# Optimization experiments

Measured on AMD Instinct MI355X. Metric: run time of the kernel, lower is better.

## Reference

```python
import jax, jax.numpy as jnp
import numpy as np

U, DP, TOPK, NH = 2, 16, 8, 2
D = 512
M = DP ** U          # 256 slots
DK = U * DP          # 32 addressing dim
BETA_MAX = 2.0


def setup_inputs():
    key = jax.random.key(0)
    ks = jax.random.split(key, 12)
    B, T = 8, 128
    s = 0.02
    return {
        "h": jax.random.normal(ks[0], (B, T, D), jnp.float32),
        "K_slots": jax.random.normal(ks[1], (B, M, D), jnp.float32) * s,
        "V_slots": jax.random.normal(ks[2], (B, M, D), jnp.float32) * s,
        "z_K": jnp.ones((B, M), jnp.float32),
        "z_V": jnp.ones((B, M), jnp.float32),
        "W_k": jax.random.normal(ks[3], (DK, D), jnp.float32) * s,
        "W_q": jax.random.normal(ks[4], (DK, D), jnp.float32) * s,
        "log_tau_w": jnp.zeros((1,), jnp.float32),
        "log_tau_r": jnp.zeros((1,), jnp.float32),
        "hh_k": jax.random.normal(ks[5], (NH, D, D), jnp.float32) * s,
        "hh_vk": jax.random.normal(ks[6], (NH, D, D), jnp.float32) * s,
        "hh_vv": jax.random.normal(ks[7], (NH, D, D), jnp.float32) * s,
        "hh_bw": jax.random.normal(ks[8], (NH, 1, D), jnp.float32) * s,
        "hh_bb": jnp.zeros((NH, 1), jnp.float32),
        "gamma": jnp.float32(1.0),
        "W_out": jax.random.normal(ks[9], (D, D), jnp.float32) * s,
        "W_gate": jax.random.normal(ks[10], (D, D), jnp.float32) * s,
    }


def _kron_address(z, log_tau):
    # z: [B, DK]; Kronecker-factored softmax address over M = DP**U slots
    B = z.shape[0]
    probs = jax.nn.softmax(z.reshape(B, U, DP) / jnp.exp(log_tau[0]), axis=-1)
    addr = probs[:, 0]
    for u in range(1, U):
        addr = (addr[:, :, None] * probs[:, u, None, :]).reshape(B, -1)
    w, idx = jax.lax.top_k(addr, TOPK)
    return idx, w


def _forward(h, K_slots, V_slots, z_K, z_V, W_k, W_q, log_tau_w, log_tau_r,
             hh_k, hh_vk, hh_vv, hh_bw, hh_bb, gamma, W_out, W_gate,
             checkpoint=False):
    B, T, _ = h.shape
    scale = D ** -0.5
    b_idx = jnp.arange(B)[:, None]
    sp_gamma = jax.nn.softplus(gamma)

    def step(carry, h_t):
        K_s, V_s, zK, zV = carry
        write_idx, write_w = _kron_address(h_t @ W_k.T, log_tau_w)
        read_idx, _ = _kron_address(h_t @ W_q.T, log_tau_r)
        # scatter write weights into dense [B, M] (top-k indices are unique)
        w_full = jnp.zeros((B, M), h_t.dtype).at[b_idx, write_idx].set(write_w)
        # PDMA decay
        decay = (1.0 - w_full) ** sp_gamma
        K_s = decay[..., None] * K_s
        V_s = decay[..., None] * V_s
        zK = decay * zK + w_full
        zV = decay * zV + w_full
        # gather active slots: [B, K, D]
        K_act = jnp.take_along_axis(K_s, write_idx[:, :, None], axis=1)
        V_act = jnp.take_along_axis(V_s, write_idx[:, :, None], axis=1)
        # Householder update chain
        for j in range(NH):
            k_j = jax.nn.silu(h_t @ hh_k[j].T)
            k_hat = k_j / jnp.maximum(
                jnp.linalg.norm(k_j, axis=-1, keepdims=True), 1e-12)
            v_kj = h_t @ hh_vk[j].T
            v_vj = h_t @ hh_vv[j].T
            beta = BETA_MAX * jax.nn.sigmoid(h_t @ hh_bw[j].T + hh_bb[j])  # [B,1]
            kh = k_hat[:, None, :]
            be = beta[:, None, :]
            K_act = K_act - be * kh * (kh * K_act).sum(-1, keepdims=True) \
                    + be * k_j[:, None, :] * v_kj[:, None, :]
            V_act = V_act - be * kh * (kh * V_act).sum(-1, keepdims=True) \
                    + be * k_j[:, None, :] * v_vj[:, None, :]
        # scatter updated slots back
        K_s = K_s.at[b_idx, write_idx].set(K_act)
        V_s = V_s.at[b_idx, write_idx].set(V_act)
        # read path
        K_read = jnp.take_along_axis(K_s, read_idx[:, :, None], axis=1)
        V_read = jnp.take_along_axis(V_s, read_idx[:, :, None], axis=1)
        zK_read = jnp.take_along_axis(zK, read_idx, axis=1)[..., None]
        zV_read = jnp.take_along_axis(zV, read_idx, axis=1)[..., None]
        K_n = K_read / zK_read
        V_n = V_read / zV_read
        rel = (K_n * h_t[:, None, :]).sum(-1)           # [B, K]
        attn = jax.nn.softmax(rel * scale, axis=-1)
        readout = (attn[..., None] * V_n).sum(1)        # [B, D]
        out = jax.nn.sigmoid(h_t @ W_gate.T) * (readout @ W_out.T)
        return (K_s, V_s, zK, zV), (out, write_idx, read_idx)

    step_fn = jax.checkpoint(step) if checkpoint else step
    (K_s, V_s, zK, zV), (outs, widx, ridx) = jax.lax.scan(
        step_fn, (K_slots, V_slots, z_K, z_V), jnp.swapaxes(h, 0, 1))
    return (jnp.swapaxes(outs, 0, 1), K_s, V_s, zK, zV, widx[-1], ridx[-1])


def reference(h, K_slots, V_slots, z_K, z_V, W_k, W_q, log_tau_w, log_tau_r,
              hh_k, hh_vk, hh_vv, hh_bw, hh_bb, gamma, W_out, W_gate):
    return _forward(h, K_slots, V_slots, z_K, z_V, W_k, W_q, log_tau_w,
                    log_tau_r, hh_k, hh_vk, hh_vv, hh_bw, hh_bb, gamma,
                    W_out, W_gate)
```

## Files before the change

kernel.cpp:

```cpp
#include <hip/hip_runtime.h>
#include <math.h>

#define D_ 512
#define M_ 256
#define T_ 128
#define B_ 8
#define TOPK_ 8
#define NH_ 2
#define BT_ (B_*T_)

__device__ __forceinline__ float wred(float v){
#pragma unroll
  for (int m = 1; m < 64; m <<= 1) v += __shfl_xor(v, m, 64);
  return v;
}
__device__ __forceinline__ float4 ld4(const float* p){ return *(const float4*)p; }
__device__ __forceinline__ void st4(float* p, float4 v){ *(float4*)p = v; }
__device__ __forceinline__ float dot4(float4 a, float4 b){
  return a.x*b.x + a.y*b.y + a.z*b.z + a.w*b.w;
}
__device__ __forceinline__ float4 scl4(float4 a, float s){
  a.x*=s; a.y*=s; a.z*=s; a.w*=s; return a;
}

template<int CTRL>
__device__ __forceinline__ float dpp_add(float x){
  int y = __builtin_amdgcn_update_dpp(0, __float_as_int(x), CTRL, 0xf, 0xf, true);
  return x + __int_as_float(y);
}
__device__ __forceinline__ float wredd(float x){
  x = dpp_add<0x111>(x);
  x = dpp_add<0x112>(x);
  x = dpp_add<0x114>(x);
  x = dpp_add<0x118>(x);
  x = dpp_add<0x142>(x);
  x = dpp_add<0x143>(x);
  return __int_as_float(__builtin_amdgcn_readlane(__float_as_int(x), 63));
}

__global__ __launch_bounds__(64) void addr_kernel(
    const float* __restrict__ h, const float* __restrict__ Wk,
    const float* __restrict__ Wq, const float* __restrict__ ltw,
    const float* __restrict__ ltr, const float* __restrict__ gammap,
    float* __restrict__ metab)
{
  const int bt = blockIdx.x;
  const int tid = threadIdx.x;
  __shared__ float p_s[64];

  const float* hrow = h + (size_t)bt*D_;
  const float* wrow = (tid < 32) ? (Wk + (size_t)tid*D_)
                                 : (Wq + (size_t)(tid-32)*D_);
  float dot = 0.f;
  for (int d = 0; d < D_; d += 4){
    float4 hv = ld4(&hrow[d]); float4 wv = ld4(&wrow[d]);
    dot += hv.x*wv.x + hv.y*wv.y + hv.z*wv.z + hv.w*wv.w;
  }
  float tau = (tid < 32) ? expf(ltw[0]) : expf(ltr[0]);
  float mx = dot;
#pragma unroll
  for (int m = 1; m < 16; m <<= 1) mx = fmaxf(mx, __shfl_xor(mx, m, 64));
  float e = expf((dot - mx)/tau);
  float sm = e;
#pragma unroll
  for (int m = 1; m < 16; m <<= 1) sm += __shfl_xor(sm, m, 64);
  p_s[tid] = e / sm;
  __syncthreads();

  const int half = tid >> 5;
  const int l = tid & 31;
  const int g0 = half*32, g1 = half*32 + 16;
  float av[8];
#pragma unroll
  for (int k = 0; k < 8; ++k){
    int x = l*8 + k;
    av[k] = p_s[g0 + (x>>4)] * p_s[g1 + (x&15)];
  }
  const float sp = log1pf(expf(gammap[0]));
  for (int r = 0; r < TOPK_; ++r){
    float bv = -1.f; int bi = 0;
#pragma unroll
    for (int k = 0; k < 8; ++k){ if (av[k] > bv){ bv = av[k]; bi = l*8+k; } }
#pragma unroll
    for (int m = 1; m < 32; m <<= 1){
      float ov = __shfl_xor(bv, m, 64); int oi = __shfl_xor(bi, m, 64);
      if (ov > bv || (ov == bv && oi < bi)){ bv = ov; bi = oi; }
    }
    if ((bi >> 3) == l) av[bi & 7] = -2.f;
    float* mp = metab + (size_t)(bt*TOPK_ + r)*4;
    if (tid == 0){
      mp[0] = __int_as_float(bi); mp[1] = bv; mp[2] = powf(1.f - bv, sp);
    }
    if (tid == 32) mp[3] = __int_as_float(bi);
  }
}

struct GemmPtrs { const float* W[6]; float* C[6]; };

__global__ __launch_bounds__(256) void gemm_nt(
    const float* __restrict__ A, GemmPtrs p,
    const float* __restrict__ zK0, const float* __restrict__ zV0,
    const float* __restrict__ metab, float2* __restrict__ zr,
    float* __restrict__ o_zK, float* __restrict__ o_zV)
{
  if (blockIdx.z == 6){
    if (blockIdx.y != 0) return;
    const int b = blockIdx.x;
    const int m = threadIdx.x;
    const float4* mb = (const float4*)metab + (size_t)b*T_*TOPK_;
    float zk = zK0[b*M_+m], zv = zV0[b*M_+m];
    float4 cur[TOPK_];
#pragma unroll
    for (int i = 0; i < TOPK_; ++i) cur[i] = mb[i];
    for (int t = 0; t < T_; ++t){
      const float4* src = mb + ((t+1 < T_) ? (t+1)*TOPK_ : t*TOPK_);
      float4 nxt[TOPK_];
#pragma unroll
      for (int i = 0; i < TOPK_; ++i) nxt[i] = src[i];
#pragma unroll
      for (int i = 0; i < TOPK_; ++i){
        bool hit = (m == __float_as_int(cur[i].x));
        float nzk = cur[i].z*zk + cur[i].y;
        float nzv = cur[i].z*zv + cur[i].y;
        zk = hit ? nzk : zk;
        zv = hit ? nzv : zv;
      }
#pragma unroll
      for (int i = 0; i < TOPK_; ++i){
        if (m == __float_as_int(cur[i].w))
          zr[(size_t)(b*T_+t)*TOPK_+i] =
              make_float2(1.0f/zk, 1.0f/zv);
      }
#pragma unroll
      for (int i = 0; i < TOPK_; ++i) cur[i] = nxt[i];
    }
    o_zK[b*M_+m] = zk; o_zV[b*M_+m] = zv;
    return;
  }

  const float* W = p.W[blockIdx.z];
  float* C = p.C[blockIdx.z];
  const int n0 = blockIdx.x * 64;
  const int m0 = blockIdx.y * 64;
  const int tid = threadIdx.x;
  __shared__ __align__(16) float As[2][16][68];
  __shared__ __align__(16) float Bs[2][16][68];
  const int r  = tid >> 2;
  const int c4 = (tid & 3) << 2;
  const int tx4 = (tid & 15) << 2;
  const int ty4 = (tid >> 4) << 2;
  float acc[4][4] = {{0.f}};

  {
    float4 av = ld4(&A[(size_t)(m0+r)*512 + c4]);
    float4 wv = ld4(&W[(size_t)(n0+r)*512 + c4]);
    As[0][c4+0][r]=av.x; As[0][c4+1][r]=av.y; As[0][c4+2][r]=av.z; As[0][c4+3][r]=av.w;
    Bs[0][c4+0][r]=wv.x; Bs[0][c4+1][r]=wv.y; Bs[0][c4+2][r]=wv.z; Bs[0][c4+3][r]=wv.w;
  }
  __syncthreads();

  for (int kc = 0, buf = 0; kc < 512; kc += 16, buf ^= 1){
    float4 av, wv;
    const bool more = (kc + 16 < 512);
    if (more){
      av = ld4(&A[(size_t)(m0+r)*512 + kc + 16 + c4]);
      wv = ld4(&W[(size_t)(n0+r)*512 + kc + 16 + c4]);
    }
#pragma unroll
    for (int k = 0; k < 16; ++k){
      float4 a  = ld4(&As[buf][k][ty4]);
      float4 bq = ld4(&Bs[buf][k][tx4]);
      acc[0][0]+=a.x*bq.x; acc[0][1]+=a.x*bq.y; acc[0][2]+=a.x*bq.z; acc[0][3]+=a.x*bq.w;
      acc[1][0]+=a.y*bq.x; acc[1][1]+=a.y*bq.y; acc[1][2]+=a.y*bq.z; acc[1][3]+=a.y*bq.w;
      acc[2][0]+=a.z*bq.x; acc[2][1]+=a.z*bq.y; acc[2][2]+=a.z*bq.z; acc[2][3]+=a.z*bq.w;
      acc[3][0]+=a.w*bq.x; acc[3][1]+=a.w*bq.y; acc[3][2]+=a.w*bq.z; acc[3][3]+=a.w*bq.w;
    }
    if (more){
      int nb = buf ^ 1;
      As[nb][c4+0][r]=av.x; As[nb][c4+1][r]=av.y; As[nb][c4+2][r]=av.z; As[nb][c4+3][r]=av.w;
      Bs[nb][c4+0][r]=wv.x; Bs[nb][c4+1][r]=wv.y; Bs[nb][c4+2][r]=wv.z; Bs[nb][c4+3][r]=wv.w;
      __syncthreads();
    }
  }
#pragma unroll
  for (int i = 0; i < 4; ++i){
    float4 cv; cv.x=acc[i][0]; cv.y=acc[i][1]; cv.z=acc[i][2]; cv.w=acc[i][3];
    st4(&C[(size_t)(m0+ty4+i)*512 + n0 + tx4], cv);
  }
}

__global__ __launch_bounds__(256) void gemm_out(
    const float* __restrict__ h, const float* __restrict__ rdo,
    const float* __restrict__ Wg, const float* __restrict__ Wo,
    float* __restrict__ C)
{
  const int n0 = blockIdx.x * 64;
  const int m0 = blockIdx.y * 64;
  const int tid = threadIdx.x;
  __shared__ __align__(16) float Ag[16][68];
  __shared__ __align__(16) float Ao[16][68];
  __shared__ __align__(16) float Bg[16][68];
  __shared__ __align__(16) float Bo[16][68];
  const int r  = tid >> 2;
  const int c4 = (tid & 3) << 2;
  const int tx4 = (tid & 15) << 2;
  const int ty4 = (tid >> 4) << 2;
  float accg[4][4] = {{0.f}};
  float acco[4][4] = {{0.f}};

  for (int kc = 0; kc < 512; kc += 16){
    float4 a1 = ld4(&h  [(size_t)(m0+r)*512 + kc + c4]);
    float4 a2 = ld4(&rdo[(size_t)(m0+r)*512 + kc + c4]);
    float4 w1 = ld4(&Wg [(size_t)(n0+r)*512 + kc + c4]);
    float4 w2 = ld4(&Wo [(size_t)(n0+r)*512 + kc + c4]);
    __syncthreads();
    Ag[c4+0][r]=a1.x; Ag[c4+1][r]=a1.y; Ag[c4+2][r]=a1.z; Ag[c4+3][r]=a1.w;
    Ao[c4+0][r]=a2.x; Ao[c4+1][r]=a2.y; Ao[c4+2][r]=a2.z; Ao[c4+3][r]=a2.w;
    Bg[c4+0][r]=w1.x; Bg[c4+1][r]=w1.y; Bg[c4+2][r]=w1.z; Bg[c4+3][r]=w1.w;
    Bo[c4+0][r]=w2.x; Bo[c4+1][r]=w2.y; Bo[c4+2][r]=w2.z; Bo[c4+3][r]=w2.w;
    __syncthreads();
#pragma unroll
    for (int k = 0; k < 16; ++k){
      float4 ag = ld4(&Ag[k][ty4]);
      float4 ao = ld4(&Ao[k][ty4]);
      float4 bg = ld4(&Bg[k][tx4]);
      float4 bo = ld4(&Bo[k][tx4]);
      accg[0][0]+=ag.x*bg.x; accg[0][1]+=ag.x*bg.y; accg[0][2]+=ag.x*bg.z; accg[0][3]+=ag.x*bg.w;
      accg[1][0]+=ag.y*bg.x; accg[1][1]+=ag.y*bg.y; accg[1][2]+=ag.y*bg.z; accg[1][3]+=ag.y*bg.w;
      accg[2][0]+=ag.z*bg.x; accg[2][1]+=ag.z*bg.y; accg[2][2]+=ag.z*bg.z; accg[2][3]+=ag.z*bg.w;
      accg[3][0]+=ag.w*bg.x; accg[3][1]+=ag.w*bg.y; accg[3][2]+=ag.w*bg.z; accg[3][3]+=ag.w*bg.w;
      acco[0][0]+=ao.x*bo.x; acco[0][1]+=ao.x*bo.y; acco[0][2]+=ao.x*bo.z; acco[0][3]+=ao.x*bo.w;
      acco[1][0]+=ao.y*bo.x; acco[1][1]+=ao.y*bo.y; acco[1][2]+=ao.y*bo.z; acco[1][3]+=ao.y*bo.w;
      acco[2][0]+=ao.z*bo.x; acco[2][1]+=ao.z*bo.y; acco[2][2]+=ao.z*bo.z; acco[2][3]+=ao.z*bo.w;
      acco[3][0]+=ao.w*bo.x; acco[3][1]+=ao.w*bo.y; acco[3][2]+=ao.w*bo.z; acco[3][3]+=ao.w*bo.w;
    }
  }
#pragma unroll
  for (int i = 0; i < 4; ++i){
    float4 cv;
    cv.x = acco[i][0] / (1.f + expf(-accg[i][0]));
    cv.y = acco[i][1] / (1.f + expf(-accg[i][1]));
    cv.z = acco[i][2] / (1.f + expf(-accg[i][2]));
    cv.w = acco[i][3] / (1.f + expf(-accg[i][3]));
    st4(&C[(size_t)(m0+ty4+i)*512 + n0 + tx4], cv);
  }
}

__global__ __launch_bounds__(256) void ew2_kernel(
    float* __restrict__ khat, float* __restrict__ kvk, float* __restrict__ kvv,
    float* __restrict__ pre2, const float* __restrict__ h,
    const float* __restrict__ hh_bw, const float* __restrict__ hh_bb)
{
  const int bt = blockIdx.x;
  const int tid = threadIdx.x;
  const int wid = tid >> 6, lane = tid & 63;
  float* k0p  = khat + (size_t)bt*D_;
  float* k1p  = khat + (size_t)BT_*D_ + (size_t)bt*D_;
  float* vk0p = kvk  + (size_t)bt*D_;
  float* vk1p = kvk  + (size_t)BT_*D_ + (size_t)bt*D_;
  float* vv0p = kvv  + (size_t)bt*D_;
  float* vv1p = kvv  + (size_t)BT_*D_ + (size_t)bt*D_;
  const float* hp  = h + (size_t)bt*D_;

  float s0[2], s1[2];
  float n0 = 0.f, n1 = 0.f, bd0 = 0.f, bd1 = 0.f;
#pragma unroll
  for (int q = 0; q < 2; ++q){
    int d = tid + q*256;
    float x0 = k0p[d], x1 = k1p[d], hv = hp[d];
    float v0 = x0 / (1.f + expf(-x0));
    float v1 = x1 / (1.f + expf(-x1));
    s0[q] = v0; s1[q] = v1;
    n0 += v0*v0; n1 += v1*v1;
    bd0 += hv*hh_bw[d]; bd1 += hv*hh_bw[D_ + d];
  }
  __shared__ float4 rb[4];
  float4 acc = make_float4(wred(n0), wred(n1), wred(bd0), wred(bd1));
  if (lane == 0) rb[wid] = acc;
  __syncthreads();
  float4 t0 = rb[0], t1 = rb[1], t2 = rb[2], t3 = rb[3];
  n0 = t0.x+t1.x+t2.x+t3.x; n1 = t0.y+t1.y+t2.y+t3.y;
  bd0 = t0.z+t1.z+t2.z+t3.z; bd1 = t0.w+t1.w+t2.w+t3.w;
  float inv0 = 1.f / fmaxf(sqrtf(n0), 1e-12f);
  float inv1 = 1.f / fmaxf(sqrtf(n1), 1e-12f);
  float be0 = 2.f / (1.f + expf(-(bd0 + hh_bb[0])));
  float be1 = 2.f / (1.f + expf(-(bd1 + hh_bb[1])));

  float c01 = 0.f, dK = 0.f, dV = 0.f;
#pragma unroll
  for (int q = 0; q < 2; ++q){
    int d = tid + q*256;
    float kh0 = s0[q]*inv0, kh1 = s1[q]*inv1;
    float u0K = s0[q]*vk0p[d], u1K = s1[q]*vk1p[d];
    float u0V = s0[q]*vv0p[d], u1V = s1[q]*vv1p[d];
    k0p[d] = kh0; k1p[d] = kh1;
    vk0p[d] = be0*u0K + be1*u1K;
    vv0p[d] = be0*u0V + be1*u1V;
    c01 += kh1*kh0; dK += kh1*u0K; dV += kh1*u0V;
  }
  __syncthreads();
  float4 acc2 = make_float4(wred(c01), wred(dK), wred(dV), 0.f);
  if (lane == 0) rb[wid] = acc2;
  __syncthreads();
  if (tid == 0){
    float4 a = rb[0], b = rb[1], c = rb[2], d = rb[3];
    pre2[(size_t)bt*8+0] = a.x+b.x+c.x+d.x;
    pre2[(size_t)bt*8+1] = a.y+b.y+c.y+d.y;
    pre2[(size_t)bt*8+2] = a.z+b.z+c.z+d.z;
    pre2[(size_t)bt*8+3] = be0;
    pre2[(size_t)bt*8+4] = be1;
  }
}

__global__ __launch_bounds__(512) void scan_kernel(
    float* __restrict__ Ks, float* __restrict__ Vs,
    const float* __restrict__ khat, const float* __restrict__ ucKp,
    const float* __restrict__ ucVp, const float* __restrict__ pre2,
    const float* __restrict__ metab, const float2* __restrict__ zr,
    const float* __restrict__ h, float* __restrict__ readout,
    float* __restrict__ o_widx, float* __restrict__ o_ridx)
{
  __shared__ __align__(16) float Vr_s[2][TOPK_][D_];
  __shared__ float2 rel2_s[2][TOPK_];

  const int b = blockIdx.x;
  const int tid = threadIdx.x;
  const int s = tid >> 6, lane = tid & 63;
  const int l4 = lane * 4;
  const float scale = 0.044194173824159216f;

  float* Ksb = Ks + (size_t)b*M_*D_;
  float* Vsb = Vs + (size_t)b*M_*D_;
  const float* kh0p = khat;
  const float* kh1p = khat + (size_t)BT_*D_;
  const float4* mb = (const float4*)metab;

  const int bt0 = b*T_;
  size_t o0 = (size_t)bt0*D_ + l4;
  float4 c_kh0a = ld4(kh0p+o0), c_kh0b = ld4(kh0p+o0+256);
  float4 c_kh1a = ld4(kh1p+o0), c_kh1b = ld4(kh1p+o0+256);
  float4 c_uKa  = ld4(ucKp+o0), c_uKb  = ld4(ucKp+o0+256);
  float4 c_uVa  = ld4(ucVp+o0), c_uVb  = ld4(ucVp+o0+256);

  float4 me   = mb[bt0*TOPK_ + s];
  float4 me_n = mb[(bt0+1)*TOPK_ + s];
  float4 pm   = ld4(&pre2[(size_t)bt0*8]);
  float  be1v = pre2[(size_t)bt0*8+4];
  float4 pm_n = ld4(&pre2[(size_t)(bt0+1)*8]);
  float  be1_n= pre2[(size_t)(bt0+1)*8+4];
  float2 zr2   = zr[(size_t)bt0*TOPK_ + s];
  float2 zr2_n = zr[(size_t)(bt0+1)*TOPK_ + s];

  int mi = __float_as_int(me.x);
  float4 K0 = ld4(&Ksb[(size_t)mi*D_ + l4]);
  float4 K1 = ld4(&Ksb[(size_t)mi*D_ + 256 + l4]);
  float4 V0 = ld4(&Vsb[(size_t)mi*D_ + l4]);
  float4 V1 = ld4(&Vsb[(size_t)mi*D_ + 256 + l4]);

#pragma unroll 2
  for (int t = 0; t < T_; ++t){
    const int bt = b*T_ + t;
    const float dec = me.z;
    const int   ri  = __float_as_int(me.w);
    mi = __float_as_int(me.x);

    const int btn  = (t+1 < T_) ? bt+1 : bt;
    const int btnn = (t+2 < T_) ? bt+2 : b*T_+T_-1;
    size_t on = (size_t)btn*D_ + l4;
    float4 n_kh0a = ld4(kh0p+on), n_kh0b = ld4(kh0p+on+256);
    float4 n_kh1a = ld4(kh1p+on), n_kh1b = ld4(kh1p+on+256);
    float4 n_uKa  = ld4(ucKp+on), n_uKb  = ld4(ucKp+on+256);
    float4 n_uVa  = ld4(ucVp+on), n_uVb  = ld4(ucVp+on+256);
    float4 HTa = ld4(h + (size_t)bt*D_ + l4);
    float4 HTb = ld4(h + (size_t)bt*D_ + 256 + l4);
    float4 me_nn = mb[btnn*TOPK_ + s];
    float4 pm_nn = ld4(&pre2[(size_t)btnn*8]);
    float  be1nn = pre2[(size_t)btnn*8+4];
    float2 zr2nn = zr[(size_t)btnn*TOPK_ + s];

    K0 = scl4(K0,dec); K1 = scl4(K1,dec);
    V0 = scl4(V0,dec); V1 = scl4(V1,dec);
    float aK = wredd(dot4(K0,c_kh0a) + dot4(K1,c_kh0b));
    float bK = wredd(dot4(K0,c_kh1a) + dot4(K1,c_kh1b));
    float aV = wredd(dot4(V0,c_kh0a) + dot4(V1,c_kh0b));
    float bV = wredd(dot4(V0,c_kh1a) + dot4(V1,c_kh1b));
    float p0K = pm.w*aK, p1K = be1v*(bK + pm.w*(pm.y - aK*pm.x));
    float p0V = pm.w*aV, p1V = be1v*(bV + pm.w*(pm.z - aV*pm.x));
    K0.x += c_uKa.x - p0K*c_kh0a.x - p1K*c_kh1a.x;
    K0.y += c_uKa.y - p0K*c_kh0a.y - p1K*c_kh1a.y;
    K0.z += c_uKa.z - p0K*c_kh0a.z - p1K*c_kh1a.z;
    K0.w += c_uKa.w - p0K*c_kh0a.w - p1K*c_kh1a.w;
    K1.x += c_uKb.x - p0K*c_kh0b.x - p1K*c_kh1b.x;
    K1.y += c_uKb.y - p0K*c_kh0b.y - p1K*c_kh1b.y;
    K1.z += c_uKb.z - p0K*c_kh0b.z - p1K*c_kh1b.z;
    K1.w += c_uKb.w - p0K*c_kh0b.w - p1K*c_kh1b.w;
    V0.x += c_uVa.x - p0V*c_kh0a.x - p1V*c_kh1a.x;
    V0.y += c_uVa.y - p0V*c_kh0a.y - p1V*c_kh1a.y;
    V0.z += c_uVa.z - p0V*c_kh0a.z - p1V*c_kh1a.z;
    V0.w += c_uVa.w - p0V*c_kh0a.w - p1V*c_kh1a.w;
    V1.x += c_uVb.x - p0V*c_kh0b.x - p1V*c_kh1b.x;
    V1.y += c_uVb.y - p0V*c_kh0b.y - p1V*c_kh1b.y;
    V1.z += c_uVb.z - p0V*c_kh0b.z - p1V*c_kh1b.z;
    V1.w += c_uVb.w - p0V*c_kh0b.w - p1V*c_kh1b.w;

    st4(&Ksb[(size_t)mi*D_ + l4], K0); st4(&Ksb[(size_t)mi*D_ + 256 + l4], K1);
    st4(&Vsb[(size_t)mi*D_ + l4], V0); st4(&Vsb[(size_t)mi*D_ + 256 + l4], V1);

    __syncthreads();

    float4 RK0 = ld4(&Ksb[(size_t)ri*D_ + l4]);
    float4 RK1 = ld4(&Ksb[(size_t)ri*D_ + 256 + l4]);
    float4 RV0 = ld4(&Vsb[(size_t)ri*D_ + l4]);
    float4 RV1 = ld4(&Vsb[(size_t)ri*D_ + 256 + l4]);
    const int mi_n = __float_as_int(me_n.x);
    float4 nK0 = ld4(&Ksb[(size_t)mi_n*D_ + l4]);
    float4 nK1 = ld4(&Ksb[(size_t)mi_n*D_ + 256 + l4]);
    float4 nV0 = ld4(&Vsb[(size_t)mi_n*D_ + l4]);
    float4 nV1 = ld4(&Vsb[(size_t)mi_n*D_ + 256 + l4]);

    if (t > 0){
      const int pp = (t-1) & 1;
      float2 rz[TOPK_];
#pragma unroll
      for (int i = 0; i < TOPK_; ++i) rz[i] = rel2_s[pp][i];
      float mx = rz[0].x;
#pragma unroll
      for (int i = 1; i < TOPK_; ++i) mx = fmaxf(mx, rz[i].x);
      float smm = 0.f, r = 0.f;
#pragma unroll
      for (int i = 0; i < TOPK_; ++i){
        float ev = __expf(rz[i].x - mx); smm += ev;
        r += ev * rz[i].y * Vr_s[pp][i][tid];
      }
      readout[(size_t)(bt-1)*D_ + tid] = r * __builtin_amdgcn_rcpf(smm);
    }

    float dt = wredd(dot4(RK0,HTa) + dot4(RK1,HTb));
    if (lane == 0)
      rel2_s[t&1][s] = make_float2(dt * scale * zr2.x, zr2.y);
    st4(&Vr_s[t&1][s][l4], RV0); st4(&Vr_s[t&1][s][256+l4], RV1);

    K0=nK0; K1=nK1; V0=nV0; V1=nV1;
    me=me_n; pm=pm_n; be1v=be1_n; zr2=zr2_n;
    me_n=me_nn; pm_n=pm_nn; be1_n=be1nn; zr2_n=zr2nn;
    c_kh0a=n_kh0a; c_kh0b=n_kh0b; c_kh1a=n_kh1a; c_kh1b=n_kh1b;
    c_uKa=n_uKa; c_uKb=n_uKb; c_uVa=n_uVa; c_uVb=n_uVb;
  }

  __syncthreads();
  {
    const int btL = b*T_ + T_ - 1;
    const int pp = (T_-1) & 1;
    float2 rz[TOPK_];
#pragma unroll
    for (int i = 0; i < TOPK_; ++i) rz[i] = rel2_s[pp][i];
    float mx = rz[0].x;
#pragma unroll
    for (int i = 1; i < TOPK_; ++i) mx = fmaxf(mx, rz[i].x);
    float smm = 0.f, r = 0.f;
#pragma unroll
    for (int i = 0; i < TOPK_; ++i){
      float ev = __expf(rz[i].x - mx); smm += ev;
      r += ev * rz[i].y * Vr_s[pp][i][tid];
    }
    readout[(size_t)btL*D_ + tid] = r * __builtin_amdgcn_rcpf(smm);

    if (tid < TOPK_){
      float4 m = mb[btL*TOPK_ + tid];
      o_widx[b*TOPK_+tid] = (float)__float_as_int(m.x);
      o_ridx[b*TOPK_+tid] = (float)__float_as_int(m.w);
    }
  }
}

extern "C" void kernel_launch(void* const* d_in, const int* in_sizes, int n_in,
                              void* d_out, int out_size, void* d_ws, size_t ws_size,
                              hipStream_t stream)
{
  (void)in_sizes; (void)n_in; (void)out_size; (void)ws_size;
  const float* h       = (const float*)d_in[0];
  const float* K_slots = (const float*)d_in[1];
  const float* V_slots = (const float*)d_in[2];
  const float* z_K     = (const float*)d_in[3];
  const float* z_V     = (const float*)d_in[4];
  const float* W_k     = (const float*)d_in[5];
  const float* W_q     = (const float*)d_in[6];
  const float* ltw     = (const float*)d_in[7];
  const float* ltr     = (const float*)d_in[8];
  const float* hh_k    = (const float*)d_in[9];
  const float* hh_vk   = (const float*)d_in[10];
  const float* hh_vv   = (const float*)d_in[11];
  const float* hh_bw   = (const float*)d_in[12];
  const float* hh_bb   = (const float*)d_in[13];
  const float* gamma   = (const float*)d_in[14];
  const float* W_out   = (const float*)d_in[15];
  const float* W_gate  = (const float*)d_in[16];

  float* out    = (float*)d_out;
  float* o_outs = out;
  float* o_Ks   = out + 524288;
  float* o_Vs   = out + 1572864;
  float* o_zK   = out + 2621440;
  float* o_zV   = out + 2623488;
  float* o_widx = out + 2625536;
  float* o_ridx = out + 2625600;

  float* ws    = (float*)d_ws;
  float* khat  = ws;
  float* kvk   = ws + 2*(size_t)BT_*D_;
  float* kvv   = kvk + 2*(size_t)BT_*D_;
  float* rdo   = kvv + 2*(size_t)BT_*D_;
  float* metab = rdo + (size_t)BT_*D_;
  float* pre2  = metab + (size_t)BT_*TOPK_*4;
  float2* zrb  = (float2*)(pre2 + (size_t)BT_*8);

  (void)hipMemcpyAsync(o_Ks, K_slots, sizeof(float)*(size_t)B_*M_*D_,
                       hipMemcpyDeviceToDevice, stream);
  (void)hipMemcpyAsync(o_Vs, V_slots, sizeof(float)*(size_t)B_*M_*D_,
                       hipMemcpyDeviceToDevice, stream);

  addr_kernel<<<BT_, 64, 0, stream>>>(h, W_k, W_q, ltw, ltr, gamma, metab);

  GemmPtrs p{};
  p.W[0] = hh_k;           p.C[0] = khat;
  p.W[1] = hh_k + 262144;  p.C[1] = khat + (size_t)BT_*D_;
  p.W[2] = hh_vk;          p.C[2] = kvk;
  p.W[3] = hh_vk + 262144; p.C[3] = kvk + (size_t)BT_*D_;
  p.W[4] = hh_vv;          p.C[4] = kvv;
  p.W[5] = hh_vv + 262144; p.C[5] = kvv + (size_t)BT_*D_;
  gemm_nt<<<dim3(8,16,7), 256, 0, stream>>>(h, p, z_K, z_V, metab, zrb,
                                            o_zK, o_zV);

  ew2_kernel<<<BT_, 256, 0, stream>>>(khat, kvk, kvv, pre2, h, hh_bw, hh_bb);

  scan_kernel<<<B_, 512, 0, stream>>>(o_Ks, o_Vs, khat, kvk, kvv,
                                      pre2, metab, zrb, h, rdo,
                                      o_widx, o_ridx);

  gemm_out<<<dim3(8,16), 256, 0, stream>>>(h, rdo, W_gate, W_out, o_outs);
}
```

Measured before the change: 464.1 us.

## Use bf16 MFMA for projection GEMMs and scalarize slot indices in scan

Replaces the shared-memory FP32 tiled GEMMs (gemm_nt and the fused gate/output gemm_out) with direct-from-global loads converted to bf16 and fed to 16x16x32 MFMA instructions, one wave per 16-column strip. It also remaps the z-recurrence block to index batch by blockIdx.y and uses readfirstlane to make per-warp slot indices scalar in the recurrent scan. The goal is to offload GEMM FLOPs to matrix cores and cut VGPR address arithmetic, at the cost of bf16 rounding of inputs and uncoalesced, non-reused global loads.

```diff
diff --git a/kernel.cpp b/kernel.cpp
--- a/kernel.cpp
+++ b/kernel.cpp
@@ -9,6 +9,9 @@
 #define NH_ 2
 #define BT_ (B_*T_)
 
+typedef __attribute__((ext_vector_type(8))) short bf8_t;
+typedef __attribute__((ext_vector_type(4))) float f4_t;
+
 __device__ __forceinline__ float wred(float v){
 #pragma unroll
   for (int m = 1; m < 64; m <<= 1) v += __shfl_xor(v, m, 64);
@@ -21,6 +24,19 @@
 }
 __device__ __forceinline__ float4 scl4(float4 a, float s){
   a.x*=s; a.y*=s; a.z*=s; a.w*=s; return a;
+}
+
+__device__ __forceinline__ short f2bf(float f){
+  unsigned u = __float_as_uint(f);
+  u += 0x7FFFu + ((u >> 16) & 1u);
+  return (short)(u >> 16);
+}
+__device__ __forceinline__ bf8_t cvt_frag(const float* p){
+  float4 x0 = ld4(p), x1 = ld4(p + 4);
+  bf8_t r;
+  r[0]=f2bf(x0.x); r[1]=f2bf(x0.y); r[2]=f2bf(x0.z); r[3]=f2bf(x0.w);
+  r[4]=f2bf(x1.x); r[5]=f2bf(x1.y); r[6]=f2bf(x1.z); r[7]=f2bf(x1.w);
+  return r;
 }
 
 template<int CTRL>
@@ -104,8 +120,8 @@
     float* __restrict__ o_zK, float* __restrict__ o_zV)
 {
   if (blockIdx.z == 6){
-    if (blockIdx.y != 0) return;
-    const int b = blockIdx.x;
+    if (blockIdx.x != 0 || blockIdx.y >= B_) return;
+    const int b = blockIdx.y;
     const int m = threadIdx.x;
     const float4* mb = (const float4*)metab + (size_t)b*T_*TOPK_;
     float zk = zK0[b*M_+m], zv = zV0[b*M_+m];
@@ -128,8 +144,7 @@
 #pragma unroll
       for (int i = 0; i < TOPK_; ++i){
         if (m == __float_as_int(cur[i].w))
-          zr[(size_t)(b*T_+t)*TOPK_+i] =
-              make_float2(1.0f/zk, 1.0f/zv);
+          zr[(size_t)(b*T_+t)*TOPK_+i] = make_float2(1.0f/zk, 1.0f/zv);
       }
 #pragma unroll
       for (int i = 0; i < TOPK_; ++i) cur[i] = nxt[i];
@@ -143,49 +158,40 @@
   const int n0 = blockIdx.x * 64;
   const int m0 = blockIdx.y * 64;
   const int tid = threadIdx.x;
-  __shared__ __align__(16) float As[2][16][68];
-  __shared__ __align__(16) float Bs[2][16][68];
-  const int r  = tid >> 2;
-  const int c4 = (tid & 3) << 2;
-  const int tx4 = (tid & 15) << 2;
-  const int ty4 = (tid >> 4) << 2;
-  float acc[4][4] = {{0.f}};
-
-  {
-    float4 av = ld4(&A[(size_t)(m0+r)*512 + c4]);
-    float4 wv = ld4(&W[(size_t)(n0+r)*512 + c4]);
-    As[0][c4+0][r]=av.x; As[0][c4+1][r]=av.y; As[0][c4+2][r]=av.z; As[0][c4+3][r]=av.w;
-    Bs[0][c4+0][r]=wv.x; Bs[0][c4+1][r]=wv.y; Bs[0][c4+2][r]=wv.z; Bs[0][c4+3][r]=wv.w;
-  }
-  __syncthreads();
-
-  for (int kc = 0, buf = 0; kc < 512; kc += 16, buf ^= 1){
-    float4 av, wv;
-    const bool more = (kc + 16 < 512);
-    if (more){
-      av = ld4(&A[(size_t)(m0+r)*512 + kc + 16 + c4]);
-      wv = ld4(&W[(size_t)(n0+r)*512 + kc + 16 + c4]);
-    }
-#pragma unroll
-    for (int k = 0; k < 16; ++k){
-      float4 a  = ld4(&As[buf][k][ty4]);
-      float4 bq = ld4(&Bs[buf][k][tx4]);
-      acc[0][0]+=a.x*bq.x; acc[0][1]+=a.x*bq.y; acc[0][2]+=a.x*bq.z; acc[0][3]+=a.x*bq.w;
-      acc[1][0]+=a.y*bq.x; acc[1][1]+=a.y*bq.y; acc[1][2]+=a.y*bq.z; acc[1][3]+=a.y*bq.w;
-      acc[2][0]+=a.z*bq.x; acc[2][1]+=a.z*bq.y; acc[2][2]+=a.z*bq.z; acc[2][3]+=a.z*bq.w;
-      acc[3][0]+=a.w*bq.x; acc[3][1]+=a.w*bq.y; acc[3][2]+=a.w*bq.z; acc[3][3]+=a.w*bq.w;
-    }
-    if (more){
-      int nb = buf ^ 1;
-      As[nb][c4+0][r]=av.x; As[nb][c4+1][r]=av.y; As[nb][c4+2][r]=av.z; As[nb][c4+3][r]=av.w;
-      Bs[nb][c4+0][r]=wv.x; Bs[nb][c4+1][r]=wv.y; Bs[nb][c4+2][r]=wv.z; Bs[nb][c4+3][r]=wv.w;
-      __syncthreads();
-    }
-  }
-#pragma unroll
-  for (int i = 0; i < 4; ++i){
-    float4 cv; cv.x=acc[i][0]; cv.y=acc[i][1]; cv.z=acc[i][2]; cv.w=acc[i][3];
-    st4(&C[(size_t)(m0+ty4+i)*512 + n0 + tx4], cv);
+  const int w = tid >> 6, lane = tid & 63;
+  const int mr = lane & 15, q = lane >> 4;
+
+  const float* a0p = A + (size_t)(m0 + mr)*512;
+  const float* a1p = a0p + (size_t)16*512;
+  const float* a2p = a1p + (size_t)16*512;
+  const float* a3p = a2p + (size_t)16*512;
+  const float* bp  = W + (size_t)(n0 + 16*w + mr)*512;
+
+  f4_t acc0 = {0.f,0.f,0.f,0.f}, acc1 = {0.f,0.f,0.f,0.f};
+  f4_t acc2 = {0.f,0.f,0.f,0.f}, acc3 = {0.f,0.f,0.f,0.f};
+
+#pragma unroll 2
+  for (int kc = 0; kc < 512; kc += 32){
+    const int ko = kc + q*8;
+    bf8_t bf = cvt_frag(bp + ko);
+    bf8_t af0 = cvt_frag(a0p + ko);
+    bf8_t af1 = cvt_frag(a1p + ko);
+    bf8_t af2 = cvt_frag(a2p + ko);
+    bf8_t af3 = cvt_frag(a3p + ko);
+    acc0 = __builtin_amdgcn_mfma_f32_16x16x32_bf16(af0, bf, acc0, 0, 0, 0);
+    acc1 = __builtin_amdgcn_mfma_f32_16x16x32_bf16(af1, bf, acc1, 0, 0, 0);
+    acc2 = __builtin_amdgcn_mfma_f32_16x16x32_bf16(af2, bf, acc2, 0, 0, 0);
+    acc3 = __builtin_amdgcn_mfma_f32_16x16x32_bf16(af3, bf, acc3, 0, 0, 0);
+  }
+
+  const int col = n0 + 16*w + mr;
+  float* c0 = C + (size_t)(m0 + q*4)*512 + col;
+#pragma unroll
+  for (int r = 0; r < 4; ++r){
+    c0[(size_t)r*512]            = acc0[r];
+    c0[(size_t)(16 + r)*512]     = acc1[r];
+    c0[(size_t)(32 + r)*512]     = acc2[r];
+    c0[(size_t)(48 + r)*512]     = acc3[r];
   }
 }
 
@@ -197,52 +203,43 @@
   const int n0 = blockIdx.x * 64;
   const int m0 = blockIdx.y * 64;
   const int tid = threadIdx.x;
-  __shared__ __align__(16) float Ag[16][68];
-  __shared__ __align__(16) float Ao[16][68];
-  __shared__ __align__(16) float Bg[16][68];
-  __shared__ __align__(16) float Bo[16][68];
-  const int r  = tid >> 2;
-  const int c4 = (tid & 3) << 2;
-  const int tx4 = (tid & 15) << 2;
-  const int ty4 = (tid >> 4) << 2;
-  float accg[4][4] = {{0.f}};
-  float acco[4][4] = {{0.f}};
-
-  for (int kc = 0; kc < 512; kc += 16){
-    float4 a1 = ld4(&h  [(size_t)(m0+r)*512 + kc + c4]);
-    float4 a2 = ld4(&rdo[(size_t)(m0+r)*512 + kc + c4]);
-    float4 w1 = ld4(&Wg [(size_t)(n0+r)*512 + kc + c4]);
-    float4 w2 = ld4(&Wo [(size_t)(n0+r)*512 + kc + c4]);
-    __syncthreads();
-    Ag[c4+0][r]=a1.x; Ag[c4+1][r]=a1.y; Ag[c4+2][r]=a1.z; Ag[c4+3][r]=a1.w;
-    Ao[c4+0][r]=a2.x; Ao[c4+1][r]=a2.y; Ao[c4+2][r]=a2.z; Ao[c4+3][r]=a2.w;
-    Bg[c4+0][r]=w1.x; Bg[c4+1][r]=w1.y; Bg[c4+2][r]=w1.z; Bg[c4+3][r]=w1.w;
-    Bo[c4+0][r]=w2.x; Bo[c4+1][r]=w2.y; Bo[c4+2][r]=w2.z; Bo[c4+3][r]=w2.w;
-    __syncthreads();
-#pragma unroll
-    for (int k = 0; k < 16; ++k){
-      float4 ag = ld4(&Ag[k][ty4]);
-      float4 ao = ld4(&Ao[k][ty4]);
-      float4 bg = ld4(&Bg[k][tx4]);
-      float4 bo = ld4(&Bo[k][tx4]);
-      accg[0][0]+=ag.x*bg.x; accg[0][1]+=ag.x*bg.y; accg[0][2]+=ag.x*bg.z; accg[0][3]+=ag.x*bg.w;
-      accg[1][0]+=ag.y*bg.x; accg[1][1]+=ag.y*bg.y; accg[1][2]+=ag.y*bg.z; accg[1][3]+=ag.y*bg.w;
-      accg[2][0]+=ag.z*bg.x; accg[2][1]+=ag.z*bg.y; accg[2][2]+=ag.z*bg.z; accg[2][3]+=ag.z*bg.w;
-      accg[3][0]+=ag.w*bg.x; accg[3][1]+=ag.w*bg.y; accg[3][2]+=ag.w*bg.z; accg[3][3]+=ag.w*bg.w;
-      acco[0][0]+=ao.x*bo.x; acco[0][1]+=ao.x*bo.y; acco[0][2]+=ao.x*bo.z; acco[0][3]+=ao.x*bo.w;
-      acco[1][0]+=ao.y*bo.x; acco[1][1]+=ao.y*bo.y; acco[1][2]+=ao.y*bo.z; acco[1][3]+=ao.y*bo.w;
-      acco[2][0]+=ao.z*bo.x; acco[2][1]+=ao.z*bo.y; acco[2][2]+=ao.z*bo.z; acco[2][3]+=ao.z*bo.w;
-      acco[3][0]+=ao.w*bo.x; acco[3][1]+=ao.w*bo.y; acco[3][2]+=ao.w*bo.z; acco[3][3]+=ao.w*bo.w;
-    }
-  }
+  const int w = tid >> 6, lane = tid & 63;
+  const int mr = lane & 15, q = lane >> 4;
+
+  const float* hp[4];  const float* op[4];
 #pragma unroll
   for (int i = 0; i < 4; ++i){
-    float4 cv;
-    cv.x = acco[i][0] / (1.f + expf(-accg[i][0]));
-    cv.y = acco[i][1] / (1.f + expf(-accg[i][1]));
-    cv.z = acco[i][2] / (1.f + expf(-accg[i][2]));
-    cv.w = acco[i][3] / (1.f + expf(-accg[i][3]));
-    st4(&C[(size_t)(m0+ty4+i)*512 + n0 + tx4], cv);
+    hp[i] = h   + (size_t)(m0 + 16*i + mr)*512;
+    op[i] = rdo + (size_t)(m0 + 16*i + mr)*512;
+  }
+  const float* gp = Wg + (size_t)(n0 + 16*w + mr)*512;
+  const float* wp = Wo + (size_t)(n0 + 16*w + mr)*512;
+
+  f4_t g[4], o[4];
+#pragma unroll
+  for (int i = 0; i < 4; ++i){ g[i] = (f4_t){0.f,0.f,0.f,0.f}; o[i] = (f4_t){0.f,0.f,0.f,0.f}; }
+
+#pragma unroll 2
+  for (int kc = 0; kc < 512; kc += 32){
+    const int ko = kc + q*8;
+    bf8_t bg = cvt_frag(gp + ko);
+    bf8_t bo = cvt_frag(wp + ko);
+#pragma unroll
+    for (int i = 0; i < 4; ++i){
+      bf8_t ah = cvt_frag(hp[i] + ko);
+      bf8_t ao = cvt_frag(op[i] + ko);
+      g[i] = __builtin_amdgcn_mfma_f32_16x16x32_bf16(ah, bg, g[i], 0, 0, 0);
+      o[i] = __builtin_amdgcn_mfma_f32_16x16x32_bf16(ao, bo, o[i], 0, 0, 0);
+    }
+  }
+
+  const int col = n0 + 16*w + mr;
+#pragma unroll
+  for (int i = 0; i < 4; ++i){
+    float* cp = C + (size_t)(m0 + 16*i + q*4)*512 + col;
+#pragma unroll
+    for (int r = 0; r < 4; ++r)
+      cp[(size_t)r*512] = o[i][r] / (1.f + expf(-g[i][r]));
   }
 }
 
@@ -351,100 +348,102 @@
   float2 zr2   = zr[(size_t)bt0*TOPK_ + s];
   float2 zr2_n = zr[(size_t)(bt0+1)*TOPK_ + s];
 
-  int mi = __float_as_int(me.x);
-  float4 K0 = ld4(&Ksb[(size_t)mi*D_ + l4]);
-  float4 K1 = ld4(&Ksb[(size_t)mi*D_ + 256 + l4]);
-  float4 V0 = ld4(&Vsb[(size_t)mi*D_ + l4]);
-  float4 V1 = ld4(&Vsb[(size_t)mi*D_ + 256 + l4]);
+  {
+    int mi0 = __builtin_amdgcn_readfirstlane(__float_as_int(me.x));
+    float4 K0 = ld4(&Ksb[(size_t)mi0*D_ + l4]);
+    float4 K1 = ld4(&Ksb[(size_t)mi0*D_ + 256 + l4]);
+    float4 V0 = ld4(&Vsb[(size_t)mi0*D_ + l4]);
+    float4 V1 = ld4(&Vsb[(size_t)mi0*D_ + 256 + l4]);
 
 #pragma unroll 2
-  for (int t = 0; t < T_; ++t){
-    const int bt = b*T_ + t;
-    const float dec = me.z;
-    const int   ri  = __float_as_int(me.w);
-    mi = __float_as_int(me.x);
-
-    const int btn  = (t+1 < T_) ? bt+1 : bt;
-    const int btnn = (t+2 < T_) ? bt+2 : b*T_+T_-1;
-    size_t on = (size_t)btn*D_ + l4;
-    float4 n_kh0a = ld4(kh0p+on), n_kh0b = ld4(kh0p+on+256);
-    float4 n_kh1a = ld4(kh1p+on), n_kh1b = ld4(kh1p+on+256);
-    float4 n_uKa  = ld4(ucKp+on), n_uKb  = ld4(ucKp+on+256);
-    float4 n_uVa  = ld4(ucVp+on), n_uVb  = ld4(ucVp+on+256);
-    float4 HTa = ld4(h + (size_t)bt*D_ + l4);
-    float4 HTb = ld4(h + (size_t)bt*D_ + 256 + l4);
-    float4 me_nn = mb[btnn*TOPK_ + s];
-    float4 pm_nn = ld4(&pre2[(size_t)btnn*8]);
-    float  be1nn = pre2[(size_t)btnn*8+4];
-    float2 zr2nn = zr[(size_t)btnn*TOPK_ + s];
-
-    K0 = scl4(K0,dec); K1 = scl4(K1,dec);
-    V0 = scl4(V0,dec); V1 = scl4(V1,dec);
-    float aK = wredd(dot4(K0,c_kh0a) + dot4(K1,c_kh0b));
-    float bK = wredd(dot4(K0,c_kh1a) + dot4(K1,c_kh1b));
-    float aV = wredd(dot4(V0,c_kh0a) + dot4(V1,c_kh0b));
-    float bV = wredd(dot4(V0,c_kh1a) + dot4(V1,c_kh1b));
-    float p0K = pm.w*aK, p1K = be1v*(bK + pm.w*(pm.y - aK*pm.x));
-    float p0V = pm.w*aV, p1V = be1v*(bV + pm.w*(pm.z - aV*pm.x));
-    K0.x += c_uKa.x - p0K*c_kh0a.x - p1K*c_kh1a.x;
-    K0.y += c_uKa.y - p0K*c_kh0a.y - p1K*c_kh1a.y;
-    K0.z += c_uKa.z - p0K*c_kh0a.z - p1K*c_kh1a.z;
-    K0.w += c_uKa.w - p0K*c_kh0a.w - p1K*c_kh1a.w;
-    K1.x += c_uKb.x - p0K*c_kh0b.x - p1K*c_kh1b.x;
-    K1.y += c_uKb.y - p0K*c_kh0b.y - p1K*c_kh1b.y;
-    K1.z += c_uKb.z - p0K*c_kh0b.z - p1K*c_kh1b.z;
-    K1.w += c_uKb.w - p0K*c_kh0b.w - p1K*c_kh1b.w;
-    V0.x += c_uVa.x - p0V*c_kh0a.x - p1V*c_kh1a.x;
-    V0.y += c_uVa.y - p0V*c_kh0a.y - p1V*c_kh1a.y;
-    V0.z += c_uVa.z - p0V*c_kh0a.z - p1V*c_kh1a.z;
-    V0.w += c_uVa.w - p0V*c_kh0a.w - p1V*c_kh1a.w;
-    V1.x += c_uVb.x - p0V*c_kh0b.x - p1V*c_kh1b.x;
-    V1.y += c_uVb.y - p0V*c_kh0b.y - p1V*c_kh1b.y;
-    V1.z += c_uVb.z - p0V*c_kh0b.z - p1V*c_kh1b.z;
-    V1.w += c_uVb.w - p0V*c_kh0b.w - p1V*c_kh1b.w;
-
-    st4(&Ksb[(size_t)mi*D_ + l4], K0); st4(&Ksb[(size_t)mi*D_ + 256 + l4], K1);
-    st4(&Vsb[(size_t)mi*D_ + l4], V0); st4(&Vsb[(size_t)mi*D_ + 256 + l4], V1);
-
-    __syncthreads();
-
-    float4 RK0 = ld4(&Ksb[(size_t)ri*D_ + l4]);
-    float4 RK1 = ld4(&Ksb[(size_t)ri*D_ + 256 + l4]);
-    float4 RV0 = ld4(&Vsb[(size_t)ri*D_ + l4]);
-    float4 RV1 = ld4(&Vsb[(size_t)ri*D_ + 256 + l4]);
-    const int mi_n = __float_as_int(me_n.x);
-    float4 nK0 = ld4(&Ksb[(size_t)mi_n*D_ + l4]);
-    float4 nK1 = ld4(&Ksb[(size_t)mi_n*D_ + 256 + l4]);
-    float4 nV0 = ld4(&Vsb[(size_t)mi_n*D_ + l4]);
-    float4 nV1 = ld4(&Vsb[(size_t)mi_n*D_ + 256 + l4]);
-
-    if (t > 0){
-      const int pp = (t-1) & 1;
-      float2 rz[TOPK_];
-#pragma unroll
-      for (int i = 0; i < TOPK_; ++i) rz[i] = rel2_s[pp][i];
-      float mx = rz[0].x;
-#pragma unroll
-      for (int i = 1; i < TOPK_; ++i) mx = fmaxf(mx, rz[i].x);
-      float smm = 0.f, r = 0.f;
-#pragma unroll
-      for (int i = 0; i < TOPK_; ++i){
-        float ev = __expf(rz[i].x - mx); smm += ev;
-        r += ev * rz[i].y * Vr_s[pp][i][tid];
+    for (int t = 0; t < T_; ++t){
+      const int bt = b*T_ + t;
+      const float dec = me.z;
+      const int ri = __builtin_amdgcn_readfirstlane(__float_as_int(me.w));
+      const int mi = __builtin_amdgcn_readfirstlane(__float_as_int(me.x));
+
+      const int btn  = (t+1 < T_) ? bt+1 : bt;
+      const int btnn = (t+2 < T_) ? bt+2 : b*T_+T_-1;
+      size_t on = (size_t)btn*D_ + l4;
+      float4 n_kh0a = ld4(kh0p+on), n_kh0b = ld4(kh0p+on+256);
+      float4 n_kh1a = ld4(kh1p+on), n_kh1b = ld4(kh1p+on+256);
+      float4 n_uKa  = ld4(ucKp+on), n_uKb  = ld4(ucKp+on+256);
+      float4 n_uVa  = ld4(ucVp+on), n_uVb  = ld4(ucVp+on+256);
+      float4 HTa = ld4(h + (size_t)bt*D_ + l4);
+      float4 HTb = ld4(h + (size_t)bt*D_ + 256 + l4);
+      float4 me_nn = mb[btnn*TOPK_ + s];
+      float4 pm_nn = ld4(&pre2[(size_t)btnn*8]);
+      float  be1nn = pre2[(size_t)btnn*8+4];
+      float2 zr2nn = zr[(size_t)btnn*TOPK_ + s];
+
+      K0 = scl4(K0,dec); K1 = scl4(K1,dec);
+      V0 = scl4(V0,dec); V1 = scl4(V1,dec);
+      float aK = wredd(dot4(K0,c_kh0a) + dot4(K1,c_kh0b));
+      float bK = wredd(dot4(K0,c_kh1a) + dot4(K1,c_kh1b));
+      float aV = wredd(dot4(V0,c_kh0a) + dot4(V1,c_kh0b));
+      float bV = wredd(dot4(V0,c_kh1a) + dot4(V1,c_kh1b));
+      float p0K = pm.w*aK, p1K = be1v*(bK + pm.w*(pm.y - aK*pm.x));
+      float p0V = pm.w*aV, p1V = be1v*(bV + pm.w*(pm.z - aV*pm.x));
+      K0.x += c_uKa.x - p0K*c_kh0a.x - p1K*c_kh1a.x;
+      K0.y += c_uKa.y - p0K*c_kh0a.y - p1K*c_kh1a.y;
+      K0.z += c_uKa.z - p0K*c_kh0a.z - p1K*c_kh1a.z;
+      K0.w += c_uKa.w - p0K*c_kh0a.w - p1K*c_kh1a.w;
+      K1.x += c_uKb.x - p0K*c_kh0b.x - p1K*c_kh1b.x;
+      K1.y += c_uKb.y - p0K*c_kh0b.y - p1K*c_kh1b.y;
+      K1.z += c_uKb.z - p0K*c_kh0b.z - p1K*c_kh1b.z;
+      K1.w += c_uKb.w - p0K*c_kh0b.w - p1K*c_kh1b.w;
+      V0.x += c_uVa.x - p0V*c_kh0a.x - p1V*c_kh1a.x;
+      V0.y += c_uVa.y - p0V*c_kh0a.y - p1V*c_kh1a.y;
+      V0.z += c_uVa.z - p0V*c_kh0a.z - p1V*c_kh1a.z;
+      V0.w += c_uVa.w - p0V*c_kh0a.w - p1V*c_kh1a.w;
+      V1.x += c_uVb.x - p0V*c_kh0b.x - p1V*c_kh1b.x;
+      V1.y += c_uVb.y - p0V*c_kh0b.y - p1V*c_kh1b.y;
+      V1.z += c_uVb.z - p0V*c_kh0b.z - p1V*c_kh1b.z;
+      V1.w += c_uVb.w - p0V*c_kh0b.w - p1V*c_kh1b.w;
+
+      st4(&Ksb[(size_t)mi*D_ + l4], K0); st4(&Ksb[(size_t)mi*D_ + 256 + l4], K1);
+      st4(&Vsb[(size_t)mi*D_ + l4], V0); st4(&Vsb[(size_t)mi*D_ + 256 + l4], V1);
+
+      __syncthreads();
+
+      float4 RK0 = ld4(&Ksb[(size_t)ri*D_ + l4]);
+      float4 RK1 = ld4(&Ksb[(size_t)ri*D_ + 256 + l4]);
+      float4 RV0 = ld4(&Vsb[(size_t)ri*D_ + l4]);
+      float4 RV1 = ld4(&Vsb[(size_t)ri*D_ + 256 + l4]);
+      const int mi_n = __builtin_amdgcn_readfirstlane(__float_as_int(me_n.x));
+      float4 nK0 = ld4(&Ksb[(size_t)mi_n*D_ + l4]);
+      float4 nK1 = ld4(&Ksb[(size_t)mi_n*D_ + 256 + l4]);
+      float4 nV0 = ld4(&Vsb[(size_t)mi_n*D_ + l4]);
+      float4 nV1 = ld4(&Vsb[(size_t)mi_n*D_ + 256 + l4]);
+
+      if (t > 0){
+        const int pp = (t-1) & 1;
+        float2 rz[TOPK_];
+#pragma unroll
+        for (int i = 0; i < TOPK_; ++i) rz[i] = rel2_s[pp][i];
+        float mx = rz[0].x;
+#pragma unroll
+        for (int i = 1; i < TOPK_; ++i) mx = fmaxf(mx, rz[i].x);
+        float smm = 0.f, r = 0.f;
+#pragma unroll
+        for (int i = 0; i < TOPK_; ++i){
+          float ev = __expf(rz[i].x - mx); smm += ev;
+          r += ev * rz[i].y * Vr_s[pp][i][tid];
+        }
+        readout[(size_t)(bt-1)*D_ + tid] = r * __builtin_amdgcn_rcpf(smm);
       }
-      readout[(size_t)(bt-1)*D_ + tid] = r * __builtin_amdgcn_rcpf(smm);
-    }
-
-    float dt = wredd(dot4(RK0,HTa) + dot4(RK1,HTb));
-    if (lane == 0)
-      rel2_s[t&1][s] = make_float2(dt * scale * zr2.x, zr2.y);
-    st4(&Vr_s[t&1][s][l4], RV0); st4(&Vr_s[t&1][s][256+l4], RV1);
-
-    K0=nK0; K1=nK1; V0=nV0; V1=nV1;
-    me=me_n; pm=pm_n; be1v=be1_n; zr2=zr2_n;
-    me_n=me_nn; pm_n=pm_nn; be1_n=be1nn; zr2_n=zr2nn;
-    c_kh0a=n_kh0a; c_kh0b=n_kh0b; c_kh1a=n_kh1a; c_kh1b=n_kh1b;
-    c_uKa=n_uKa; c_uKb=n_uKb; c_uVa=n_uVa; c_uVb=n_uVb;
+
+      float dt = wredd(dot4(RK0,HTa) + dot4(RK1,HTb));
+      if (lane == 0)
+        rel2_s[t&1][s] = make_float2(dt * scale * zr2.x, zr2.y);
+      st4(&Vr_s[t&1][s][l4], RV0); st4(&Vr_s[t&1][s][256+l4], RV1);
+
+      K0=nK0; K1=nK1; V0=nV0; V1=nV1;
+      me=me_n; pm=pm_n; be1v=be1_n; zr2=zr2_n;
+      me_n=me_nn; pm_n=pm_nn; be1_n=be1nn; zr2_n=zr2nn;
+      c_kh0a=n_kh0a; c_kh0b=n_kh0b; c_kh1a=n_kh1a; c_kh1b=n_kh1b;
+      c_uKa=n_uKa; c_uKb=n_uKb; c_uVa=n_uVa; c_uVb=n_uVb;
+    }
   }
 
   __syncthreads();
```

Measured after the change: 503.9 us. 8.6% more time.
